# Optimization experiments

Measured on AMD Instinct MI355X. Metric: run time of the kernel, lower is better.

Reference implementation:

```python
import jax, jax.numpy as jnp
import numpy as np

D_X, N_LAYERS, N_HEADS, D_OUT = 1024, 4, 16, 1024
D_H = D_X // N_HEADS
LN_EPS = 1e-5


def _layernorm(x, g, b):
    mu = jnp.mean(x, axis=-1, keepdims=True)
    var = jnp.var(x, axis=-1, keepdims=True)
    return (x - mu) * jax.lax.rsqrt(var + LN_EPS) * g + b


def setup_inputs() -> dict:
    key = jax.random.key(0)
    ks = jax.random.split(key, 12)
    s = 0.02
    inp = {
        "x": jax.random.normal(ks[0], (4, 1024, D_X), dtype=jnp.float32),
        # per-layer, per-head K/V projections (Q is unused by the original math)
        "Wk": jax.random.normal(ks[1], (N_LAYERS, N_HEADS, D_X, D_H), dtype=jnp.float32) * s,
        "bk": jnp.zeros((N_LAYERS, N_HEADS, D_H), dtype=jnp.float32),
        "Wv": jax.random.normal(ks[2], (N_LAYERS, N_HEADS, D_X, D_H), dtype=jnp.float32) * s,
        "bv": jnp.zeros((N_LAYERS, N_HEADS, D_H), dtype=jnp.float32),
        # per-layer FFN linear
        "Wl": jax.random.normal(ks[3], (N_LAYERS, D_X, D_X), dtype=jnp.float32) * s,
        "bl": jnp.zeros((N_LAYERS, D_X), dtype=jnp.float32),
        # per-layer LayerNorm params
        "g1": jnp.ones((N_LAYERS, D_X), dtype=jnp.float32),
        "b1": jnp.zeros((N_LAYERS, D_X), dtype=jnp.float32),
        "g2": jnp.ones((N_LAYERS, D_X), dtype=jnp.float32),
        "b2": jnp.zeros((N_LAYERS, D_X), dtype=jnp.float32),
        # output projection
        "Wo": jax.random.normal(ks[4], (D_X, D_OUT), dtype=jnp.float32) * s,
        "bo": jnp.zeros((D_OUT,), dtype=jnp.float32),
    }
    return inp


def reference(x, Wk, bk, Wv, bv, Wl, bl, g1, b1, g2, b2, Wo, bo):
    B, S, _ = x.shape
    scale = 1.0 / np.sqrt(D_H).astype(np.float32)
    for l in range(N_LAYERS):
        # batched across heads instead of the original per-head Python loop
        K = jnp.einsum("bsd,hdk->bhsk", x, Wk[l]) + bk[l][None, :, None, :]
        V = jnp.einsum("bsd,hdk->bhsk", x, Wv[l]) + bv[l][None, :, None, :]
        # faithful quirk: logits = K @ V^T (Q is never used in the source)
        logits = jnp.einsum("bhsk,bhtk->bhst", K, V) * scale
        attn = jnp.einsum("bhst,bhtk->bhsk", jax.nn.softmax(logits, axis=-1), V)
        attn = attn.transpose(0, 2, 1, 3).reshape(B, S, D_X)  # concat heads
        x = _layernorm(x + attn, g1[l], b1[l])
        ff = jax.nn.relu(jnp.einsum("bsd,de->bse", x, Wl[l]) + bl[l])
        x = _layernorm(x + ff, g2[l], b2[l])
    return jnp.einsum("bsd,do->bso", x, Wo) + bo
```

## Files before the change

### kernel.cpp

```cpp
#include <hip/hip_runtime.h>

typedef unsigned short u16;
typedef unsigned int u32;
typedef __attribute__((ext_vector_type(4))) float f32x4;
typedef __attribute__((ext_vector_type(8))) short short8;

#if __has_builtin(__builtin_amdgcn_exp2f)
#define EXP2(x) __builtin_amdgcn_exp2f(x)
#else
#define EXP2(x) exp2f(x)
#endif

#define SCALEK 0.18033688011112042f

__device__ __forceinline__ u16 f2b(float f) {
    unsigned u = __float_as_uint(f);
    u += 0x7fff + ((u >> 16) & 1);
    return (u16)(u >> 16);
}
__device__ __forceinline__ float b2f(u16 v) {
    return __uint_as_float(((unsigned)v) << 16);
}
__device__ __forceinline__ int swz(int byteoff) {
    return byteoff ^ (((byteoff >> 7) & 7) << 4);
}
__device__ __forceinline__ void gl16(const u16* g, u16* l) {
    __builtin_amdgcn_global_load_lds(
        (const __attribute__((address_space(1))) unsigned*)(g),
        (__attribute__((address_space(3))) unsigned*)(l), 16, 0, 0);
}
__device__ __forceinline__ u32 cvtpk(float lo, float hi) {
    u32 r;
    asm("v_cvt_pk_bf16_f32 %0, %1, %2" : "=v"(r) : "v"(lo), "v"(hi));
    return r;
}
__device__ __forceinline__ void plswap(u32& a, u32& b) {
    asm("v_permlane32_swap_b32 %0, %1" : "+v"(a), "+v"(b));
    asm("v_permlane16_swap_b32 %0, %1" : "+v"(a), "+v"(b));
}

__global__ __launch_bounds__(256) void pack_wkv_t(const float* __restrict__ W,
                                                  u16* __restrict__ out, int voff) {
    __shared__ float tile[32][33];
    int z = blockIdx.z; int l = z >> 4, h = z & 15;
    const float* ip = W + (size_t)z * 1024 * 64;
    u16* op = out + (size_t)l * 2048 * 1024 + (size_t)(voff + h * 64) * 1024;
    int tx = threadIdx.x & 31, ty = threadIdx.x >> 5;
    int d0 = blockIdx.y * 32, k0 = blockIdx.x * 32;
#pragma unroll
    for (int j = 0; j < 32; j += 8)
        tile[ty + j][tx] = ip[(size_t)(d0 + ty + j) * 64 + k0 + tx];
    __syncthreads();
#pragma unroll
    for (int j = 0; j < 32; j += 8)
        op[(size_t)(k0 + ty + j) * 1024 + d0 + tx] = f2b(tile[tx][ty + j]);
}

__global__ __launch_bounds__(256) void transpose_cvt(const float* __restrict__ in,
                                                     u16* __restrict__ out, int R, int C) {
    __shared__ float tile[32][33];
    const float* ip = in + (size_t)blockIdx.z * R * C;
    u16* op = out + (size_t)blockIdx.z * R * C;
    int tx = threadIdx.x & 31, ty = threadIdx.x >> 5;
    int r0 = blockIdx.y * 32, c0 = blockIdx.x * 32;
#pragma unroll
    for (int j = 0; j < 32; j += 8)
        tile[ty + j][tx] = ip[(size_t)(r0 + ty + j) * C + c0 + tx];
    __syncthreads();
#pragma unroll
    for (int j = 0; j < 32; j += 8)
        op[(size_t)(c0 + ty + j) * R + r0 + tx] = f2b(tile[tx][ty + j]);
}

__global__ __launch_bounds__(256) void cvt_bf16(const float* __restrict__ in,
                                                u16* __restrict__ out, int n) {
    int i = (blockIdx.x * 256 + threadIdx.x) * 4;
    if (i >= n) return;
    float4 v = *(const float4*)&in[i];
    ushort4 o = {f2b(v.x), f2b(v.y), f2b(v.z), f2b(v.w)};
    *(ushort4*)&out[i] = o;
}

template <int EPI, int BN>
__global__ __launch_bounds__(256) void gemm_bt(const u16* __restrict__ A,
                                               const u16* __restrict__ B,
                                               const float* __restrict__ bias1,
                                               const float* __restrict__ bias2, int split,
                                               void* __restrict__ Cv,
                                               u16* __restrict__ VTout,
                                               int M, int N, int K) {
    constexpr int NB = BN / 32;
    constexpr int BCH = BN * 4;
    __shared__ __align__(16) u16 lA[2][512 * 8];
    __shared__ __align__(16) u16 lB[2][BCH * 8];
    const int t = threadIdx.x;
    const int lane = t & 63, w = t >> 6;
    const int wr = w >> 1, wc = w & 1;
    const int g = lane >> 4, r = lane & 15;
    const int m0 = blockIdx.y * 128, n0 = blockIdx.x * BN;

    const int c1 = w * 64 + lane;
    const int c2 = 256 + c1;
    const u16* Ap1 = A + (size_t)(m0 + (c1 & 127)) * K + (c1 >> 7) * 8;
    const u16* Ap2 = A + (size_t)(m0 + (c2 & 127)) * K + (c2 >> 7) * 8;
    const u16* Bp1 = B + (size_t)(n0 + (c1 & (BN - 1))) * K + (c1 / BN) * 8;
    const u16* Bp2 = B + (size_t)(n0 + (c2 & (BN - 1))) * K + (c2 / BN) * 8;

    f32x4 zero4 = {0.f, 0.f, 0.f, 0.f};
    f32x4 acc[4][NB];
#pragma unroll
    for (int m = 0; m < 4; ++m)
#pragma unroll
        for (int n = 0; n < NB; ++n) acc[m][n] = zero4;

#define GSTAGE(bufi, k0)                                        \
    do {                                                        \
        gl16(Ap1 + (k0), &lA[bufi][(w * 64) * 8]);              \
        gl16(Ap2 + (k0), &lA[bufi][(256 + w * 64) * 8]);        \
        gl16(Bp1 + (k0), &lB[bufi][(w * 64) * 8]);              \
        if constexpr (BN == 128)                                \
            gl16(Bp2 + (k0), &lB[bufi][(256 + w * 64) * 8]);    \
    } while (0)

    GSTAGE(0, 0);
    __syncthreads();
    const int nk = K >> 5;
    for (int kt = 0; kt < nk; ++kt) {
        const int cur = kt & 1;
        if (kt + 1 < nk) GSTAGE(cur ^ 1, (kt + 1) * 32);
        short8 af[4], bf[NB];
#pragma unroll
        for (int m = 0; m < 4; ++m)
            af[m] = *(const short8*)&lA[cur][(g * 128 + wr * 64 + m * 16 + r) * 8];
#pragma unroll
        for (int n = 0; n < NB; ++n)
            bf[n] = *(const short8*)&lB[cur][(g * BN + wc * (BN / 2) + n * 16 + r) * 8];
#pragma unroll
        for (int m = 0; m < 4; ++m)
#pragma unroll
            for (int n = 0; n < NB; ++n)
                acc[m][n] = __builtin_amdgcn_mfma_f32_16x16x32_bf16(af[m], bf[n], acc[m][n], 0, 0, 0);
        __syncthreads();
    }
#undef GSTAGE

#pragma unroll
    for (int m = 0; m < 4; ++m) {
        int row = m0 + wr * 64 + m * 16 + g * 4;
#pragma unroll
        for (int n = 0; n < NB; ++n) {
            int col = n0 + wc * (BN / 2) + n * 16 + r;
            float bv_ = (col < split) ? bias1[col] : bias2[col - split];
            if (EPI == 0) {
                float sc = (col < split) ? SCALEK : 1.0f;
                ushort4 qv;
                qv.x = f2b((acc[m][n][0] + bv_) * sc);
                qv.y = f2b((acc[m][n][1] + bv_) * sc);
                qv.z = f2b((acc[m][n][2] + bv_) * sc);
                qv.w = f2b((acc[m][n][3] + bv_) * sc);
                u16* Cb = (u16*)Cv;
                Cb[(size_t)(row + 0) * N + col] = qv.x;
                Cb[(size_t)(row + 1) * N + col] = qv.y;
                Cb[(size_t)(row + 2) * N + col] = qv.z;
                Cb[(size_t)(row + 3) * N + col] = qv.w;
                if (col >= split) {
                    int d = col - split, b_ = row >> 10, s = row & 1023;
                    *(ushort4*)&VTout[(((size_t)(b_ * 16) + (d >> 6)) * 64 + (d & 63)) * 1024 + s] = qv;
                }
            } else if (EPI == 1) {
                u16* Cb = (u16*)Cv;
#pragma unroll
                for (int i = 0; i < 4; ++i)
                    Cb[(size_t)(row + i) * N + col] = f2b(fmaxf(acc[m][n][i] + bv_, 0.f));
            } else {
#pragma unroll
                for (int i = 0; i < 4; ++i)
                    ((float*)Cv)[(size_t)(row + i) * N + col] = acc[m][n][i] + bv_;
            }
        }
    }
}

__global__ __launch_bounds__(512) void attn_kernel(const u16* __restrict__ KV,
                                                   const u16* __restrict__ VT,
                                                   u16* __restrict__ Out) {
    __shared__ __align__(16) u16 kt[2][512 * 8];
    __shared__ __align__(16) u16 vt[2][512 * 8];
    const int t = threadIdx.x;
    const int lane = t & 63, w = t >> 6;
    const int g = lane >> 4, r = lane & 15;
    const int d0 = blockIdx.x;
    const int q = d0 >> 3;
    const int bh = (d0 & 7) * 8 + (q >> 3), qb = q & 7;
    const int h = bh & 15, b = bh >> 4;
    const u16* Kbase = KV + (size_t)b * 1024 * 2048 + h * 64;
    const u16* Vbase = Kbase + 1024;
    const u16* VTbase = VT + ((size_t)(b * 16 + h)) * 64 * 1024;

    const int qrow = qb * 128 + w * 16 + r;
    const short8 qf0 = *(const short8*)&Kbase[(size_t)qrow * 2048 + g * 8];
    const short8 qf1 = *(const short8*)&Kbase[(size_t)qrow * 2048 + 32 + g * 8];

    const int row = t >> 3;
    const int colu = (((t & 7) * 16) ^ ((row & 7) << 4)) >> 1;
    const u16* Ksrc = Vbase + (size_t)row * 2048 + colu;
    const u16* Vsrc = VTbase + (size_t)row * 1024 + colu;

#define STAGE(bufi, t0)                                   \
    do {                                                  \
        gl16(Ksrc + (size_t)(t0) * 2048, &kt[bufi][(w * 64) * 8]); \
        gl16(Vsrc + (t0), &vt[bufi][(w * 64) * 8]);       \
    } while (0)

    STAGE(0, 0);

    float m = -1e30f, l = 0.f;
    f32x4 zero4 = {0.f, 0.f, 0.f, 0.f};
    f32x4 oacc[4];
#pragma unroll
    for (int n = 0; n < 4; ++n) oacc[n] = zero4;
    const int cbase = (lane & 48) | (g << 2);
    __syncthreads();

    for (int tt = 0; tt < 16; ++tt) {
        const int cur = tt & 1;
        if (tt < 15) STAGE(cur ^ 1, (tt + 1) * 64);
        const char* kbuf = (const char*)&kt[cur][0];
        const char* vbuf = (const char*)&vt[cur][0];

        f32x4 sfT[4];
#pragma unroll
        for (int n = 0; n < 4; ++n) sfT[n] = zero4;
#pragma unroll
        for (int ks = 0; ks < 2; ++ks) {
            const short8 qf = ks ? qf1 : qf0;
#pragma unroll
            for (int n = 0; n < 4; ++n) {
                short8 kf = *(const short8*)(kbuf + swz((n * 16 + r) * 128 + ks * 64 + g * 16));
                sfT[n] = __builtin_amdgcn_mfma_f32_16x16x32_bf16(kf, qf, sfT[n], 0, 0, 0);
            }
        }
        float rm = fmaxf(fmaxf(sfT[0][0], sfT[0][1]), fmaxf(sfT[0][2], sfT[0][3]));
        float r1 = fmaxf(fmaxf(sfT[1][0], sfT[1][1]), fmaxf(sfT[1][2], sfT[1][3]));
        float r2 = fmaxf(fmaxf(sfT[2][0], sfT[2][1]), fmaxf(sfT[2][2], sfT[2][3]));
        float r3 = fmaxf(fmaxf(sfT[3][0], sfT[3][1]), fmaxf(sfT[3][2], sfT[3][3]));
        rm = fmaxf(fmaxf(rm, r1), fmaxf(r2, r3));
        rm = fmaxf(rm, __shfl_xor(rm, 16, 64));
        rm = fmaxf(rm, __shfl_xor(rm, 32, 64));
        if (!__all(rm <= m + 8.f)) {
            float mn = fmaxf(m, rm);
            float cc = EXP2(m - mn);
            m = mn;
            l *= cc;
#pragma unroll
            for (int i = 0; i < 4; ++i) {
                float ci = __shfl(cc, cbase + i, 64);
#pragma unroll
                for (int n = 0; n < 4; ++n) oacc[n][i] *= ci;
            }
        }
        float rs = 0.f;
#pragma unroll
        for (int n = 0; n < 4; ++n)
#pragma unroll
            for (int i = 0; i < 4; ++i) {
                float p = EXP2(sfT[n][i] - m);
                sfT[n][i] = p;
                rs += p;
            }
        rs += __shfl_xor(rs, 16, 64);
        rs += __shfl_xor(rs, 32, 64);
        l += rs;
        u32 wpk[4][2];
#pragma unroll
        for (int n = 0; n < 4; ++n) {
            wpk[n][0] = cvtpk(sfT[n][0], sfT[n][1]);
            wpk[n][1] = cvtpk(sfT[n][2], sfT[n][3]);
        }
#pragma unroll
        for (int ks = 0; ks < 2; ++ks) {
            u32 a0 = wpk[2 * ks][0], a2 = wpk[2 * ks + 1][0];
            plswap(a0, a2);
            u32 a1 = wpk[2 * ks][1], a3 = wpk[2 * ks + 1][1];
            plswap(a1, a3);
            uint4 av;
            av.x = a0; av.y = a1; av.z = a2; av.w = a3;
            union { uint4 u; short8 s; } uc;
            uc.u = av;
            const short8 af = uc.s;
#pragma unroll
            for (int n = 0; n < 4; ++n) {
                short8 vf = *(const short8*)(vbuf + swz((n * 16 + r) * 128 + ks * 64 + g * 16));
                oacc[n] = __builtin_amdgcn_mfma_f32_16x16x32_bf16(af, vf, oacc[n], 0, 0, 0);
            }
        }
        __syncthreads();
    }
#undef STAGE

#pragma unroll
    for (int i = 0; i < 4; ++i) {
        float li = 1.f / __shfl(l, cbase + i, 64);
        int orow = b * 1024 + qb * 128 + w * 16 + g * 4 + i;
#pragma unroll
        for (int n = 0; n < 4; ++n)
            Out[(size_t)orow * 1024 + h * 64 + n * 16 + r] = f2b(oacc[n][i] * li);
    }
}

__global__ __launch_bounds__(256) void ln_kernel(const u16* __restrict__ xin,
                                                 const u16* __restrict__ addin,
                                                 const float* __restrict__ gamma,
                                                 const float* __restrict__ beta,
                                                 u16* __restrict__ xbout) {
    const int row = blockIdx.x, t = threadIdx.x;
    const size_t base = (size_t)row * 1024;
    ushort4 xu = *(const ushort4*)&xin[base + t * 4];
    ushort4 au = *(const ushort4*)&addin[base + t * 4];
    float v0 = b2f(xu.x) + b2f(au.x), v1 = b2f(xu.y) + b2f(au.y);
    float v2 = b2f(xu.z) + b2f(au.z), v3 = b2f(xu.w) + b2f(au.w);
    float s = v0 + v1 + v2 + v3;
    __shared__ float red[4];
    const int lane = t & 63, w = t >> 6;
#pragma unroll
    for (int off = 32; off; off >>= 1) s += __shfl_xor(s, off, 64);
    if (lane == 0) red[w] = s;
    __syncthreads();
    float mean = (red[0] + red[1] + red[2] + red[3]) * (1.f / 1024.f);
    __syncthreads();
    float d0 = v0 - mean, d1 = v1 - mean, d2 = v2 - mean, d3 = v3 - mean;
    float sq = d0 * d0 + d1 * d1 + d2 * d2 + d3 * d3;
#pragma unroll
    for (int off = 32; off; off >>= 1) sq += __shfl_xor(sq, off, 64);
    if (lane == 0) red[w] = sq;
    __syncthreads();
    float var = (red[0] + red[1] + red[2] + red[3]) * (1.f / 1024.f);
    float rstd = rsqrtf(var + 1e-5f);
    float4 gv = *(const float4*)&gamma[t * 4];
    float4 bv = *(const float4*)&beta[t * 4];
    ushort4 o;
    o.x = f2b(d0 * rstd * gv.x + bv.x);
    o.y = f2b(d1 * rstd * gv.y + bv.y);
    o.z = f2b(d2 * rstd * gv.z + bv.z);
    o.w = f2b(d3 * rstd * gv.w + bv.w);
    *(ushort4*)&xbout[base + t * 4] = o;
}

extern "C" void kernel_launch(void* const* d_in, const int* in_sizes, int n_in,
                              void* d_out, int out_size, void* d_ws, size_t ws_size,
                              hipStream_t stream) {
    const float* x  = (const float*)d_in[0];
    const float* Wk = (const float*)d_in[1];
    const float* bk = (const float*)d_in[2];
    const float* Wv = (const float*)d_in[3];
    const float* bv = (const float*)d_in[4];
    const float* Wl = (const float*)d_in[5];
    const float* bl = (const float*)d_in[6];
    const float* g1 = (const float*)d_in[7];
    const float* b1 = (const float*)d_in[8];
    const float* g2 = (const float*)d_in[9];
    const float* b2 = (const float*)d_in[10];
    const float* Wo = (const float*)d_in[11];
    const float* bo = (const float*)d_in[12];

    char* ws = (char*)d_ws;
    u16* Wkvb = (u16*)ws;  ws += (size_t)4 * 2048 * 1024 * 2;
    u16* Wlb  = (u16*)ws;  ws += (size_t)4 * 1024 * 1024 * 2;
    u16* Wob  = (u16*)ws;  ws += (size_t)1024 * 1024 * 2;
    u16* xb   = (u16*)ws;  ws += (size_t)4096 * 1024 * 2;
    u16* KVb  = (u16*)ws;  ws += (size_t)4096 * 2048 * 2;
    u16* VTb  = (u16*)ws;  ws += (size_t)4096 * 1024 * 2;
    u16* tmpb = (u16*)ws;  ws += (size_t)4096 * 1024 * 2;

    pack_wkv_t<<<dim3(2, 32, 64), 256, 0, stream>>>(Wk, Wkvb, 0);
    pack_wkv_t<<<dim3(2, 32, 64), 256, 0, stream>>>(Wv, Wkvb, 1024);
    transpose_cvt<<<dim3(32, 32, 4), 256, 0, stream>>>(Wl, Wlb, 1024, 1024);
    transpose_cvt<<<dim3(32, 32, 1), 256, 0, stream>>>(Wo, Wob, 1024, 1024);
    cvt_bf16<<<dim3(4096), 256, 0, stream>>>(x, xb, 4096 * 1024);

    for (int l = 0; l < 4; ++l) {
        gemm_bt<0, 128><<<dim3(16, 32), 256, 0, stream>>>(
            xb, Wkvb + (size_t)l * 2048 * 1024, bk + l * 1024, bv + l * 1024, 1024,
            (void*)KVb, VTb, 4096, 2048, 1024);
        attn_kernel<<<dim3(512), 512, 0, stream>>>(KVb, VTb, tmpb);
        ln_kernel<<<dim3(4096), 256, 0, stream>>>(
            xb, tmpb, g1 + l * 1024, b1 + l * 1024, xb);
        gemm_bt<1, 64><<<dim3(16, 32), 256, 0, stream>>>(
            xb, Wlb + (size_t)l * 1024 * 1024, bl + l * 1024, bl + l * 1024, 1024,
            (void*)tmpb, nullptr, 4096, 1024, 1024);
        ln_kernel<<<dim3(4096), 256, 0, stream>>>(
            xb, tmpb, g2 + l * 1024, b2 + l * 1024, xb);
    }
    gemm_bt<2, 64><<<dim3(16, 32), 256, 0, stream>>>(
        xb, Wob, bo, bo, 1024, d_out, nullptr, 4096, 1024, 1024);
}
```

Before: 502.5 us.

## Triple-buffer LDS staging in GEMM and attention with one barrier per iteration

```diff
diff --git a/kernel.cpp b/kernel.cpp
--- a/kernel.cpp
+++ b/kernel.cpp
@@ -90,9 +90,9 @@
                                                u16* __restrict__ VTout,
                                                int M, int N, int K) {
     constexpr int NB = BN / 32;
-    constexpr int BCH = BN * 4;
-    __shared__ __align__(16) u16 lA[2][512 * 8];
-    __shared__ __align__(16) u16 lB[2][BCH * 8];
+    constexpr int NLD = (BN == 128) ? 4 : 3;
+    __shared__ __align__(16) u16 lA[3][512 * 8];
+    __shared__ __align__(16) u16 lB[3][BN * 4 * 8];
     const int t = threadIdx.x;
     const int lane = t & 63, w = t >> 6;
     const int wr = w >> 1, wc = w & 1;
@@ -123,11 +123,18 @@
     } while (0)
 
     GSTAGE(0, 0);
-    __syncthreads();
+    GSTAGE(1, 32);
     const int nk = K >> 5;
+    int cur = 0, pf = 2;
     for (int kt = 0; kt < nk; ++kt) {
-        const int cur = kt & 1;
-        if (kt + 1 < nk) GSTAGE(cur ^ 1, (kt + 1) * 32);
+        if (kt < nk - 1) {
+            asm volatile("s_waitcnt vmcnt(%0)" :: "i"(NLD) : "memory");
+        } else {
+            asm volatile("s_waitcnt vmcnt(0)" ::: "memory");
+        }
+        __builtin_amdgcn_s_barrier();
+        __builtin_amdgcn_sched_barrier(0);
+        if (kt + 2 < nk) GSTAGE(pf, (kt + 2) * 32);
         short8 af[4], bf[NB];
 #pragma unroll
         for (int m = 0; m < 4; ++m)
@@ -140,7 +147,8 @@
 #pragma unroll
             for (int n = 0; n < NB; ++n)
                 acc[m][n] = __builtin_amdgcn_mfma_f32_16x16x32_bf16(af[m], bf[n], acc[m][n], 0, 0, 0);
-        __syncthreads();
+        cur = (cur == 2) ? 0 : cur + 1;
+        pf = (pf == 2) ? 0 : pf + 1;
     }
 #undef GSTAGE
 
@@ -184,8 +192,8 @@
 __global__ __launch_bounds__(512) void attn_kernel(const u16* __restrict__ KV,
                                                    const u16* __restrict__ VT,
                                                    u16* __restrict__ Out) {
-    __shared__ __align__(16) u16 kt[2][512 * 8];
-    __shared__ __align__(16) u16 vt[2][512 * 8];
+    __shared__ __align__(16) u16 kt[3][512 * 8];
+    __shared__ __align__(16) u16 vt[3][512 * 8];
     const int t = threadIdx.x;
     const int lane = t & 63, w = t >> 6;
     const int g = lane >> 4, r = lane & 15;
@@ -213,6 +221,7 @@
     } while (0)
 
     STAGE(0, 0);
+    STAGE(1, 64);
 
     float m = -1e30f, l = 0.f;
     f32x4 zero4 = {0.f, 0.f, 0.f, 0.f};
@@ -220,11 +229,17 @@
 #pragma unroll
     for (int n = 0; n < 4; ++n) oacc[n] = zero4;
     const int cbase = (lane & 48) | (g << 2);
-    __syncthreads();
-
+
+    int cur = 0, pf = 2;
     for (int tt = 0; tt < 16; ++tt) {
-        const int cur = tt & 1;
-        if (tt < 15) STAGE(cur ^ 1, (tt + 1) * 64);
+        if (tt < 15) {
+            asm volatile("s_waitcnt vmcnt(2)" ::: "memory");
+        } else {
+            asm volatile("s_waitcnt vmcnt(0)" ::: "memory");
+        }
+        __builtin_amdgcn_s_barrier();
+        __builtin_amdgcn_sched_barrier(0);
+        if (tt + 2 < 16) STAGE(pf, (tt + 2) * 64);
         const char* kbuf = (const char*)&kt[cur][0];
         const char* vbuf = (const char*)&vt[cur][0];
 
@@ -294,7 +309,8 @@
                 oacc[n] = __builtin_amdgcn_mfma_f32_16x16x32_bf16(af, vf, oacc[n], 0, 0, 0);
             }
         }
-        __syncthreads();
+        cur = (cur == 2) ? 0 : cur + 1;
+        pf = (pf == 2) ? 0 : pf + 1;
     }
 #undef STAGE
 
```

Measured after the change: 513.1 us. 2.1% more time.

## Replace LDS-staged GEMM with direct-global MFMA GEMM and halve attention blocks

Applied to the files above, without the earlier changes.

```diff
diff --git a/kernel.cpp b/kernel.cpp
--- a/kernel.cpp
+++ b/kernel.cpp
@@ -81,75 +81,59 @@
     *(ushort4*)&out[i] = o;
 }
 
-template <int EPI, int BN>
-__global__ __launch_bounds__(256) void gemm_bt(const u16* __restrict__ A,
-                                               const u16* __restrict__ B,
-                                               const float* __restrict__ bias1,
-                                               const float* __restrict__ bias2, int split,
-                                               void* __restrict__ Cv,
-                                               u16* __restrict__ VTout,
-                                               int M, int N, int K) {
-    constexpr int NB = BN / 32;
-    constexpr int BCH = BN * 4;
-    __shared__ __align__(16) u16 lA[2][512 * 8];
-    __shared__ __align__(16) u16 lB[2][BCH * 8];
+template <int EPI, int WM, int WN, int GXLOG, int K>
+__global__ __launch_bounds__(256, 4) void gemm_direct(const u16* __restrict__ A,
+                                                      const u16* __restrict__ B,
+                                                      const float* __restrict__ bias1,
+                                                      const float* __restrict__ bias2,
+                                                      int split, void* __restrict__ Cv,
+                                                      u16* __restrict__ VTout, int N) {
+    constexpr int NA = WM / 16, NB = WN / 16;
     const int t = threadIdx.x;
     const int lane = t & 63, w = t >> 6;
     const int wr = w >> 1, wc = w & 1;
     const int g = lane >> 4, r = lane & 15;
-    const int m0 = blockIdx.y * 128, n0 = blockIdx.x * BN;
-
-    const int c1 = w * 64 + lane;
-    const int c2 = 256 + c1;
-    const u16* Ap1 = A + (size_t)(m0 + (c1 & 127)) * K + (c1 >> 7) * 8;
-    const u16* Ap2 = A + (size_t)(m0 + (c2 & 127)) * K + (c2 >> 7) * 8;
-    const u16* Bp1 = B + (size_t)(n0 + (c1 & (BN - 1))) * K + (c1 / BN) * 8;
-    const u16* Bp2 = B + (size_t)(n0 + (c2 & (BN - 1))) * K + (c2 / BN) * 8;
+    const int nwg = gridDim.x;
+    const int wg = (blockIdx.x & 7) * (nwg >> 3) + (blockIdx.x >> 3);
+    const int bx = wg & ((1 << GXLOG) - 1), by = wg >> GXLOG;
+    const int m0 = by * (2 * WM), n0 = bx * (2 * WN);
+
+    const u16* Ab[NA];
+    const u16* Bb[NB];
+#pragma unroll
+    for (int m = 0; m < NA; ++m)
+        Ab[m] = A + (size_t)(m0 + wr * WM + m * 16 + r) * K + g * 8;
+#pragma unroll
+    for (int n = 0; n < NB; ++n)
+        Bb[n] = B + (size_t)(n0 + wc * WN + n * 16 + r) * K + g * 8;
 
     f32x4 zero4 = {0.f, 0.f, 0.f, 0.f};
-    f32x4 acc[4][NB];
-#pragma unroll
-    for (int m = 0; m < 4; ++m)
+    f32x4 acc[NA][NB];
+#pragma unroll
+    for (int m = 0; m < NA; ++m)
 #pragma unroll
         for (int n = 0; n < NB; ++n) acc[m][n] = zero4;
 
-#define GSTAGE(bufi, k0)                                        \
-    do {                                                        \
-        gl16(Ap1 + (k0), &lA[bufi][(w * 64) * 8]);              \
-        gl16(Ap2 + (k0), &lA[bufi][(256 + w * 64) * 8]);        \
-        gl16(Bp1 + (k0), &lB[bufi][(w * 64) * 8]);              \
-        if constexpr (BN == 128)                                \
-            gl16(Bp2 + (k0), &lB[bufi][(256 + w * 64) * 8]);    \
-    } while (0)
-
-    GSTAGE(0, 0);
-    __syncthreads();
-    const int nk = K >> 5;
-    for (int kt = 0; kt < nk; ++kt) {
-        const int cur = kt & 1;
-        if (kt + 1 < nk) GSTAGE(cur ^ 1, (kt + 1) * 32);
-        short8 af[4], bf[NB];
-#pragma unroll
-        for (int m = 0; m < 4; ++m)
-            af[m] = *(const short8*)&lA[cur][(g * 128 + wr * 64 + m * 16 + r) * 8];
-#pragma unroll
-        for (int n = 0; n < NB; ++n)
-            bf[n] = *(const short8*)&lB[cur][(g * BN + wc * (BN / 2) + n * 16 + r) * 8];
-#pragma unroll
-        for (int m = 0; m < 4; ++m)
+#pragma unroll 4
+    for (int k0 = 0; k0 < K; k0 += 32) {
+        short8 af[NA], bf[NB];
+#pragma unroll
+        for (int m = 0; m < NA; ++m) af[m] = *(const short8*)(Ab[m] + k0);
+#pragma unroll
+        for (int n = 0; n < NB; ++n) bf[n] = *(const short8*)(Bb[n] + k0);
+#pragma unroll
+        for (int m = 0; m < NA; ++m)
 #pragma unroll
             for (int n = 0; n < NB; ++n)
                 acc[m][n] = __builtin_amdgcn_mfma_f32_16x16x32_bf16(af[m], bf[n], acc[m][n], 0, 0, 0);
-        __syncthreads();
-    }
-#undef GSTAGE
-
-#pragma unroll
-    for (int m = 0; m < 4; ++m) {
-        int row = m0 + wr * 64 + m * 16 + g * 4;
+    }
+
+#pragma unroll
+    for (int m = 0; m < NA; ++m) {
+        int row = m0 + wr * WM + m * 16 + g * 4;
 #pragma unroll
         for (int n = 0; n < NB; ++n) {
-            int col = n0 + wc * (BN / 2) + n * 16 + r;
+            int col = n0 + wc * WN + n * 16 + r;
             float bv_ = (col < split) ? bias1[col] : bias2[col - split];
             if (EPI == 0) {
                 float sc = (col < split) ? SCALEK : 1.0f;
@@ -181,7 +165,7 @@
     }
 }
 
-__global__ __launch_bounds__(512) void attn_kernel(const u16* __restrict__ KV,
+__global__ __launch_bounds__(256) void attn_kernel(const u16* __restrict__ KV,
                                                    const u16* __restrict__ VT,
                                                    u16* __restrict__ Out) {
     __shared__ __align__(16) u16 kt[2][512 * 8];
@@ -190,26 +174,31 @@
     const int lane = t & 63, w = t >> 6;
     const int g = lane >> 4, r = lane & 15;
     const int d0 = blockIdx.x;
-    const int q = d0 >> 3;
-    const int bh = (d0 & 7) * 8 + (q >> 3), qb = q & 7;
+    const int hi = d0 & 7, qb = (d0 >> 3) & 15, mid = d0 >> 7;
+    const int bh = hi * 8 + mid;
     const int h = bh & 15, b = bh >> 4;
     const u16* Kbase = KV + (size_t)b * 1024 * 2048 + h * 64;
     const u16* Vbase = Kbase + 1024;
     const u16* VTbase = VT + ((size_t)(b * 16 + h)) * 64 * 1024;
 
-    const int qrow = qb * 128 + w * 16 + r;
+    const int qrow = qb * 64 + w * 16 + r;
     const short8 qf0 = *(const short8*)&Kbase[(size_t)qrow * 2048 + g * 8];
     const short8 qf1 = *(const short8*)&Kbase[(size_t)qrow * 2048 + 32 + g * 8];
 
-    const int row = t >> 3;
-    const int colu = (((t & 7) * 16) ^ ((row & 7) << 4)) >> 1;
-    const u16* Ksrc = Vbase + (size_t)row * 2048 + colu;
-    const u16* Vsrc = VTbase + (size_t)row * 1024 + colu;
-
-#define STAGE(bufi, t0)                                   \
-    do {                                                  \
-        gl16(Ksrc + (size_t)(t0) * 2048, &kt[bufi][(w * 64) * 8]); \
-        gl16(Vsrc + (t0), &vt[bufi][(w * 64) * 8]);       \
+    const int row1 = t >> 3;
+    const int row2 = 32 + row1;
+    const int colu = (((t & 7) * 16) ^ ((row1 & 7) << 4)) >> 1;
+    const u16* Ks1 = Vbase + (size_t)row1 * 2048 + colu;
+    const u16* Ks2 = Vbase + (size_t)row2 * 2048 + colu;
+    const u16* Vs1 = VTbase + (size_t)row1 * 1024 + colu;
+    const u16* Vs2 = VTbase + (size_t)row2 * 1024 + colu;
+
+#define STAGE(bufi, t0)                                              \
+    do {                                                             \
+        gl16(Ks1 + (size_t)(t0) * 2048, &kt[bufi][(w * 64) * 8]);    \
+        gl16(Ks2 + (size_t)(t0) * 2048, &kt[bufi][(256 + w * 64) * 8]); \
+        gl16(Vs1 + (t0), &vt[bufi][(w * 64) * 8]);                   \
+        gl16(Vs2 + (t0), &vt[bufi][(256 + w * 64) * 8]);             \
     } while (0)
 
     STAGE(0, 0);
@@ -301,7 +290,7 @@
 #pragma unroll
     for (int i = 0; i < 4; ++i) {
         float li = 1.f / __shfl(l, cbase + i, 64);
-        int orow = b * 1024 + qb * 128 + w * 16 + g * 4 + i;
+        int orow = b * 1024 + qb * 64 + w * 16 + g * 4 + i;
 #pragma unroll
         for (int n = 0; n < 4; ++n)
             Out[(size_t)orow * 1024 + h * 64 + n * 16 + r] = f2b(oacc[n][i] * li);
@@ -379,18 +368,18 @@
     cvt_bf16<<<dim3(4096), 256, 0, stream>>>(x, xb, 4096 * 1024);
 
     for (int l = 0; l < 4; ++l) {
-        gemm_bt<0, 128><<<dim3(16, 32), 256, 0, stream>>>(
+        gemm_direct<0, 64, 32, 5, 1024><<<dim3(1024), 256, 0, stream>>>(
             xb, Wkvb + (size_t)l * 2048 * 1024, bk + l * 1024, bv + l * 1024, 1024,
-            (void*)KVb, VTb, 4096, 2048, 1024);
-        attn_kernel<<<dim3(512), 512, 0, stream>>>(KVb, VTb, tmpb);
+            (void*)KVb, VTb, 2048);
+        attn_kernel<<<dim3(1024), 256, 0, stream>>>(KVb, VTb, tmpb);
         ln_kernel<<<dim3(4096), 256, 0, stream>>>(
             xb, tmpb, g1 + l * 1024, b1 + l * 1024, xb);
-        gemm_bt<1, 64><<<dim3(16, 32), 256, 0, stream>>>(
+        gemm_direct<1, 32, 32, 4, 1024><<<dim3(1024), 256, 0, stream>>>(
             xb, Wlb + (size_t)l * 1024 * 1024, bl + l * 1024, bl + l * 1024, 1024,
-            (void*)tmpb, nullptr, 4096, 1024, 1024);
+            (void*)tmpb, nullptr, 1024);
         ln_kernel<<<dim3(4096), 256, 0, stream>>>(
             xb, tmpb, g2 + l * 1024, b2 + l * 1024, xb);
     }
-    gemm_bt<2, 64><<<dim3(16, 32), 256, 0, stream>>>(
-        xb, Wob, bo, bo, 1024, d_out, nullptr, 4096, 1024, 1024);
-}
+    gemm_direct<2, 32, 32, 4, 1024><<<dim3(1024), 256, 0, stream>>>(
+        xb, Wob, bo, bo, 1024, d_out, nullptr, 1024);
+}
```

Result: slower. 887.1 us (+76.5%).

## Retile GEMMs with K-step 64, smaller tiles and XCD-aware block remapping

Applied to the files above, without the earlier changes.

```diff
diff --git a/kernel.cpp b/kernel.cpp
--- a/kernel.cpp
+++ b/kernel.cpp
@@ -38,6 +38,7 @@
     asm("v_permlane32_swap_b32 %0, %1" : "+v"(a), "+v"(b));
     asm("v_permlane16_swap_b32 %0, %1" : "+v"(a), "+v"(b));
 }
+#define MFMA16(a, b, c) __builtin_amdgcn_mfma_f32_16x16x32_bf16((a), (b), (c), 0, 0, 0)
 
 __global__ __launch_bounds__(256) void pack_wkv_t(const float* __restrict__ W,
                                                   u16* __restrict__ out, int voff) {
@@ -81,75 +82,89 @@
     *(ushort4*)&out[i] = o;
 }
 
-template <int EPI, int BN>
-__global__ __launch_bounds__(256) void gemm_bt(const u16* __restrict__ A,
-                                               const u16* __restrict__ B,
-                                               const float* __restrict__ bias1,
-                                               const float* __restrict__ bias2, int split,
-                                               void* __restrict__ Cv,
-                                               u16* __restrict__ VTout,
-                                               int M, int N, int K) {
-    constexpr int NB = BN / 32;
-    constexpr int BCH = BN * 4;
-    __shared__ __align__(16) u16 lA[2][512 * 8];
-    __shared__ __align__(16) u16 lB[2][BCH * 8];
+template <int EPI, int TM, int TN, int GXLOG>
+__global__ __launch_bounds__(256) void gemm_bt2(const u16* __restrict__ A,
+                                                const u16* __restrict__ B,
+                                                const float* __restrict__ bias1,
+                                                const float* __restrict__ bias2, int split,
+                                                void* __restrict__ Cv,
+                                                u16* __restrict__ VTout, int N) {
+    constexpr int K = 1024;
+    constexpr int MR = TM / 32, NR = TN / 32;
+    constexpr int NLA = TM * 8 / 256;
+    constexpr int NLB = TN * 8 / 256;
+    constexpr int L2TM = (TM == 128) ? 7 : 6;
+    constexpr int L2TN = (TN == 128) ? 7 : 6;
+    __shared__ __align__(16) u16 lA[2][TM * 64];
+    __shared__ __align__(16) u16 lB[2][TN * 64];
     const int t = threadIdx.x;
     const int lane = t & 63, w = t >> 6;
     const int wr = w >> 1, wc = w & 1;
     const int g = lane >> 4, r = lane & 15;
-    const int m0 = blockIdx.y * 128, n0 = blockIdx.x * BN;
-
-    const int c1 = w * 64 + lane;
-    const int c2 = 256 + c1;
-    const u16* Ap1 = A + (size_t)(m0 + (c1 & 127)) * K + (c1 >> 7) * 8;
-    const u16* Ap2 = A + (size_t)(m0 + (c2 & 127)) * K + (c2 >> 7) * 8;
-    const u16* Bp1 = B + (size_t)(n0 + (c1 & (BN - 1))) * K + (c1 / BN) * 8;
-    const u16* Bp2 = B + (size_t)(n0 + (c2 & (BN - 1))) * K + (c2 / BN) * 8;
+    const int nwg = gridDim.x;
+    const int wg = ((int)blockIdx.x & 7) * (nwg >> 3) + ((int)blockIdx.x >> 3);
+    const int bx = wg & ((1 << GXLOG) - 1), by = wg >> GXLOG;
+    const int m0 = by * TM, n0 = bx * TN;
+
+    const u16* sA[NLA];
+    const u16* sB[NLB];
+#pragma unroll
+    for (int j = 0; j < NLA; ++j) {
+        int c = j * 256 + t;
+        sA[j] = A + (size_t)(m0 + (c & (TM - 1))) * K + (c >> L2TM) * 8;
+    }
+#pragma unroll
+    for (int j = 0; j < NLB; ++j) {
+        int c = j * 256 + t;
+        sB[j] = B + (size_t)(n0 + (c & (TN - 1))) * K + (c >> L2TN) * 8;
+    }
 
     f32x4 zero4 = {0.f, 0.f, 0.f, 0.f};
-    f32x4 acc[4][NB];
-#pragma unroll
-    for (int m = 0; m < 4; ++m)
-#pragma unroll
-        for (int n = 0; n < NB; ++n) acc[m][n] = zero4;
-
-#define GSTAGE(bufi, k0)                                        \
-    do {                                                        \
-        gl16(Ap1 + (k0), &lA[bufi][(w * 64) * 8]);              \
-        gl16(Ap2 + (k0), &lA[bufi][(256 + w * 64) * 8]);        \
-        gl16(Bp1 + (k0), &lB[bufi][(w * 64) * 8]);              \
-        if constexpr (BN == 128)                                \
-            gl16(Bp2 + (k0), &lB[bufi][(256 + w * 64) * 8]);    \
+    f32x4 acc[MR][NR];
+#pragma unroll
+    for (int m = 0; m < MR; ++m)
+#pragma unroll
+        for (int n = 0; n < NR; ++n) acc[m][n] = zero4;
+
+#define GSTAGE(bufi, k0)                                                \
+    do {                                                                \
+        _Pragma("unroll") for (int j = 0; j < NLA; ++j)                 \
+            gl16(sA[j] + (k0), &lA[bufi][(j * 256 + w * 64) * 8]);      \
+        _Pragma("unroll") for (int j = 0; j < NLB; ++j)                 \
+            gl16(sB[j] + (k0), &lB[bufi][(j * 256 + w * 64) * 8]);      \
     } while (0)
 
     GSTAGE(0, 0);
     __syncthreads();
-    const int nk = K >> 5;
+    constexpr int nk = K / 64;
     for (int kt = 0; kt < nk; ++kt) {
         const int cur = kt & 1;
-        if (kt + 1 < nk) GSTAGE(cur ^ 1, (kt + 1) * 32);
-        short8 af[4], bf[NB];
-#pragma unroll
-        for (int m = 0; m < 4; ++m)
-            af[m] = *(const short8*)&lA[cur][(g * 128 + wr * 64 + m * 16 + r) * 8];
-#pragma unroll
-        for (int n = 0; n < NB; ++n)
-            bf[n] = *(const short8*)&lB[cur][(g * BN + wc * (BN / 2) + n * 16 + r) * 8];
-#pragma unroll
-        for (int m = 0; m < 4; ++m)
-#pragma unroll
-            for (int n = 0; n < NB; ++n)
-                acc[m][n] = __builtin_amdgcn_mfma_f32_16x16x32_bf16(af[m], bf[n], acc[m][n], 0, 0, 0);
+        if (kt + 1 < nk) GSTAGE(cur ^ 1, (kt + 1) * 64);
+#pragma unroll
+        for (int ks = 0; ks < 2; ++ks) {
+            short8 af[MR], bf[NR];
+#pragma unroll
+            for (int m = 0; m < MR; ++m)
+                af[m] = *(const short8*)&lA[cur][((ks * 4 + g) * TM + wr * (TM / 2) + m * 16 + r) * 8];
+#pragma unroll
+            for (int n = 0; n < NR; ++n)
+                bf[n] = *(const short8*)&lB[cur][((ks * 4 + g) * TN + wc * (TN / 2) + n * 16 + r) * 8];
+#pragma unroll
+            for (int m = 0; m < MR; ++m)
+#pragma unroll
+                for (int n = 0; n < NR; ++n)
+                    acc[m][n] = MFMA16(af[m], bf[n], acc[m][n]);
+        }
         __syncthreads();
     }
 #undef GSTAGE
 
 #pragma unroll
-    for (int m = 0; m < 4; ++m) {
-        int row = m0 + wr * 64 + m * 16 + g * 4;
-#pragma unroll
-        for (int n = 0; n < NB; ++n) {
-            int col = n0 + wc * (BN / 2) + n * 16 + r;
+    for (int m = 0; m < MR; ++m) {
+        int row = m0 + wr * (TM / 2) + m * 16 + g * 4;
+#pragma unroll
+        for (int n = 0; n < NR; ++n) {
+            int col = n0 + wc * (TN / 2) + n * 16 + r;
             float bv_ = (col < split) ? bias1[col] : bias2[col - split];
             if (EPI == 0) {
                 float sc = (col < split) ? SCALEK : 1.0f;
@@ -206,10 +221,10 @@
     const u16* Ksrc = Vbase + (size_t)row * 2048 + colu;
     const u16* Vsrc = VTbase + (size_t)row * 1024 + colu;
 
-#define STAGE(bufi, t0)                                   \
-    do {                                                  \
+#define STAGE(bufi, t0)                                            \
+    do {                                                           \
         gl16(Ksrc + (size_t)(t0) * 2048, &kt[bufi][(w * 64) * 8]); \
-        gl16(Vsrc + (t0), &vt[bufi][(w * 64) * 8]);       \
+        gl16(Vsrc + (t0), &vt[bufi][(w * 64) * 8]);                \
     } while (0)
 
     STAGE(0, 0);
@@ -237,7 +252,7 @@
 #pragma unroll
             for (int n = 0; n < 4; ++n) {
                 short8 kf = *(const short8*)(kbuf + swz((n * 16 + r) * 128 + ks * 64 + g * 16));
-                sfT[n] = __builtin_amdgcn_mfma_f32_16x16x32_bf16(kf, qf, sfT[n], 0, 0, 0);
+                sfT[n] = MFMA16(kf, qf, sfT[n]);
             }
         }
         float rm = fmaxf(fmaxf(sfT[0][0], sfT[0][1]), fmaxf(sfT[0][2], sfT[0][3]));
@@ -291,7 +306,7 @@
 #pragma unroll
             for (int n = 0; n < 4; ++n) {
                 short8 vf = *(const short8*)(vbuf + swz((n * 16 + r) * 128 + ks * 64 + g * 16));
-                oacc[n] = __builtin_amdgcn_mfma_f32_16x16x32_bf16(af, vf, oacc[n], 0, 0, 0);
+                oacc[n] = MFMA16(af, vf, oacc[n]);
             }
         }
         __syncthreads();
@@ -379,18 +394,18 @@
     cvt_bf16<<<dim3(4096), 256, 0, stream>>>(x, xb, 4096 * 1024);
 
     for (int l = 0; l < 4; ++l) {
-        gemm_bt<0, 128><<<dim3(16, 32), 256, 0, stream>>>(
+        gemm_bt2<0, 128, 64, 5><<<dim3(1024), 256, 0, stream>>>(
             xb, Wkvb + (size_t)l * 2048 * 1024, bk + l * 1024, bv + l * 1024, 1024,
-            (void*)KVb, VTb, 4096, 2048, 1024);
+            (void*)KVb, VTb, 2048);
         attn_kernel<<<dim3(512), 512, 0, stream>>>(KVb, VTb, tmpb);
         ln_kernel<<<dim3(4096), 256, 0, stream>>>(
             xb, tmpb, g1 + l * 1024, b1 + l * 1024, xb);
-        gemm_bt<1, 64><<<dim3(16, 32), 256, 0, stream>>>(
+        gemm_bt2<1, 64, 64, 4><<<dim3(1024), 256, 0, stream>>>(
             xb, Wlb + (size_t)l * 1024 * 1024, bl + l * 1024, bl + l * 1024, 1024,
-            (void*)tmpb, nullptr, 4096, 1024, 1024);
+            (void*)tmpb, nullptr, 1024);
         ln_kernel<<<dim3(4096), 256, 0, stream>>>(
             xb, tmpb, g2 + l * 1024, b2 + l * 1024, xb);
     }
-    gemm_bt<2, 64><<<dim3(16, 32), 256, 0, stream>>>(
-        xb, Wob, bo, bo, 1024, d_out, nullptr, 4096, 1024, 1024);
-}
+    gemm_bt2<2, 64, 64, 4><<<dim3(1024), 256, 0, stream>>>(
+        xb, Wob, bo, bo, 1024, d_out, nullptr, 1024);
+}
```

Result: slower. 629.7 us (+25.3%).
